# Optimization experiments

Measured on AMD Instinct MI355X. Metric: run time of the kernel, lower is better.

Reference implementation:

```python
import jax, jax.numpy as jnp
import numpy as np

D_MODEL = 512
HEADS = 8
D_FF = 1024
EPS = 1e-5


def layer_norm(x, gamma, beta):
    mu = jnp.mean(x, axis=-1, keepdims=True)
    var = jnp.mean(jnp.square(x - mu), axis=-1, keepdims=True)
    return (x - mu) * jax.lax.rsqrt(var + EPS) * gamma + beta


def mha(q, k, v, mask=None):
    # q,k,v: [B, S, D]; no input/output projections in the original module
    B, Sq, D = q.shape
    Sk = k.shape[1]
    dk = D // HEADS
    qh = q.reshape(B, Sq, HEADS, dk).transpose(0, 2, 1, 3)  # [B,H,Sq,dk]
    kh = k.reshape(B, Sk, HEADS, dk).transpose(0, 2, 1, 3)
    vh = v.reshape(B, Sk, HEADS, dk).transpose(0, 2, 1, 3)
    scores = jnp.einsum('bhqd,bhkd->bhqk', qh, kh) / np.sqrt(dk).astype(q.dtype)
    if mask is not None:
        scores = jnp.where(mask == 0, jnp.asarray(-1e9, scores.dtype), scores)
    attn = jax.nn.softmax(scores, axis=-1)  # dropout is identity in eval mode
    out = jnp.einsum('bhqk,bhkd->bhqd', attn, vh)
    return out.transpose(0, 2, 1, 3).reshape(B, Sq, D)


def setup_inputs() -> dict:
    key = jax.random.key(0)
    ks = jax.random.split(key, 8)
    B, S = 4, 2048
    x = jax.random.normal(ks[0], (B, S, D_MODEL), dtype=jnp.float32)
    encoder_output = jax.random.normal(ks[1], (B, S, D_MODEL), dtype=jnp.float32)
    mask = jax.random.randint(ks[2], (B, 1, S, S), 0, 2, dtype=jnp.int32)
    params = {
        'ln1_g': jnp.ones((D_MODEL,), jnp.float32), 'ln1_b': jnp.zeros((D_MODEL,), jnp.float32),
        'ln2_g': jnp.ones((D_MODEL,), jnp.float32), 'ln2_b': jnp.zeros((D_MODEL,), jnp.float32),
        'ln3_g': jnp.ones((D_MODEL,), jnp.float32), 'ln3_b': jnp.zeros((D_MODEL,), jnp.float32),
        'W1': jax.random.normal(ks[3], (D_MODEL, D_FF), jnp.float32) * (1.0 / np.sqrt(D_MODEL)),
        'b1': jnp.zeros((D_FF,), jnp.float32),
        'W2': jax.random.normal(ks[4], (D_FF, D_MODEL), jnp.float32) * (1.0 / np.sqrt(D_FF)),
        'b2': jnp.zeros((D_MODEL,), jnp.float32),
    }
    return {'x': x, 'encoder_output': encoder_output, 'mask': mask, **params}


def reference(x, encoder_output, mask, ln1_g, ln1_b, ln2_g, ln2_b, ln3_g, ln3_b, W1, b1, W2, b2):
    # pre-norm masked self-attention + residual (dropout = identity, eval mode)
    x1 = layer_norm(x, ln1_g, ln1_b)
    x = x + mha(x1, x1, x1, mask)
    # pre-norm cross-attention + residual
    x1 = layer_norm(x, ln2_g, ln2_b)
    x = x + mha(x1, encoder_output, encoder_output, None)
    # pre-norm FFN + residual
    x1 = layer_norm(x, ln3_g, ln3_b)
    h = jax.nn.relu(x1 @ W1 + b1)
    x = x + (h @ W2 + b2)
    return x
```

## Files before the change

kernel.cpp:

```cpp
#include <hip/hip_runtime.h>
#include <hip/hip_bf16.h>

#define D_MODEL 512
#define HEADS   8
#define DK      64
#define D_FF    1024
#define SEQ     2048
#define BATCH   4
#define NTOK    (BATCH*SEQ)
#define NELEM   (NTOK*D_MODEL)

#define QSCALE  0.18033688011112042f
#define MFIX    40.0f

typedef __attribute__((ext_vector_type(8))) short bf8_t;
typedef __attribute__((ext_vector_type(4))) short bf4_t;
typedef __attribute__((ext_vector_type(4))) float f4_t;

#define GLD16(gp, lp) __builtin_amdgcn_global_load_lds( \
    (const __attribute__((address_space(1))) void*)(gp), \
    (__attribute__((address_space(3))) void*)(lp), 16, 0, 0)

__device__ __forceinline__ float ldf(const void* p, size_t i, int f32) {
    return f32 ? ((const float*)p)[i] : __bfloat162float(((const __hip_bfloat16*)p)[i]);
}
__device__ __forceinline__ short f2bf(float f) {
    union { __hip_bfloat16 h; short s; } u; u.h = __float2bfloat16(f); return u.s;
}
__device__ __forceinline__ float bf2f(short s) {
    return __uint_as_float(((unsigned)(unsigned short)s) << 16);
}
__device__ __forceinline__ unsigned fbits(float f) { return __float_as_uint(f); }

__device__ __forceinline__ float fast_exp2(float x) {
    float r; asm("v_exp_f32 %0, %1" : "=v"(r) : "v"(x)); return r;
}

__global__ void detect_k(const uint4* __restrict__ w, int* __restrict__ flags) {
    __shared__ int found;
    if (threadIdx.x == 0) found = 0;
    __syncthreads();
    int hit = 0;
    for (int i = threadIdx.x; i < 4096; i += 256) {
        uint4 u = w[i];
        if (((u.x & 0x7F80u) == 0x7F80u) || ((u.y & 0x7F80u) == 0x7F80u) ||
            ((u.z & 0x7F80u) == 0x7F80u) || ((u.w & 0x7F80u) == 0x7F80u)) hit = 1;
    }
    if (hit) atomicOr(&found, 1);
    __syncthreads();
    if (threadIdx.x == 0) flags[0] = found ? 1 : 0;
}

__device__ __forceinline__ void transpose_body(const void* src, __hip_bfloat16* dst,
                                               int K, int N, int bxi, int byi, int f32,
                                               __hip_bfloat16 (*t)[33]) {
    int bx = bxi * 32, by = byi * 32;
    int tx = threadIdx.x & 31, ty = threadIdx.x >> 5;
    #pragma unroll
    for (int j = 0; j < 32; j += 8)
        t[ty + j][tx] = __float2bfloat16(ldf(src, (size_t)(by + ty + j) * N + bx + tx, f32));
    __syncthreads();
    #pragma unroll
    for (int j = 0; j < 32; j += 8)
        dst[(size_t)(bx + ty + j) * K + by + tx] = t[tx][ty + j];
}

__global__ __launch_bounds__(256)
void prep_k(const void* __restrict__ enc, const int* __restrict__ mask,
            const void* __restrict__ W1, const void* __restrict__ W2,
            const void* __restrict__ x,
            const void* __restrict__ ln1g, const void* __restrict__ ln1b,
            const void* __restrict__ ln2g, const void* __restrict__ ln2b,
            const void* __restrict__ ln3g, const void* __restrict__ ln3b,
            const void* __restrict__ b1,   const void* __restrict__ b2,
            const int* __restrict__ flagp,
            __hip_bfloat16* __restrict__ bufE, unsigned* __restrict__ mb,
            __hip_bfloat16* __restrict__ W1T, __hip_bfloat16* __restrict__ W2T,
            float* __restrict__ bufX, __hip_bfloat16* __restrict__ bufQ,
            __hip_bfloat16* __restrict__ pbuf) {
    __shared__ __hip_bfloat16 t[32][33];
    int f32 = *flagp;
    int bid = blockIdx.x;
    if (bid < 4096) {
        int i = bid * 256 + threadIdx.x;
        if (f32) {
            float4 a = ((const float4*)enc)[i];
            bf4_t o = { f2bf(a.x), f2bf(a.y), f2bf(a.z), f2bf(a.w) };
            ((bf4_t*)bufE)[i] = o;
        } else {
            ((bf4_t*)bufE)[i] = ((const bf4_t*)enc)[i];
        }
    } else if (bid < 6144) {
        int row  = (bid - 4096) * 4 + (threadIdx.x >> 6);
        int lane = threadIdx.x & 63;
        const int* mr = mask + (size_t)row * SEQ;
        for (int it = 0; it < SEQ/64; it++) {
            unsigned long long bal = __ballot(mr[it*64 + lane] != 0);
            if (lane == 0)  mb[(size_t)row*(SEQ/32) + it*2]     = (unsigned)bal;
            if (lane == 32) mb[(size_t)row*(SEQ/32) + it*2 + 1] = (unsigned)(bal >> 32);
        }
    } else if (bid < 6656) {
        int lb = bid - 6144;
        transpose_body(W1, W1T, D_MODEL, D_FF, lb & 31, lb >> 5, f32, t);
    } else if (bid < 7168) {
        int lb = bid - 6656;
        transpose_body(W2, W2T, D_FF, D_MODEL, lb & 15, lb >> 4, f32, t);
    } else if (bid < 9216) {
        int row  = (bid - 7168) * 4 + (threadIdx.x >> 6);
        int lane = threadIdx.x & 63;
        size_t base = (size_t)row * D_MODEL;
        float v[8];
        if (f32) {
            const float4* xp = (const float4*)((const float*)x + base);
            float4 a = xp[lane], b4 = xp[64 + lane];
            v[0]=a.x; v[1]=a.y; v[2]=a.z; v[3]=a.w;
            v[4]=b4.x; v[5]=b4.y; v[6]=b4.z; v[7]=b4.w;
        } else {
            const bf4_t* xp = (const bf4_t*)((const __hip_bfloat16*)x + base);
            bf4_t a = xp[lane], b4 = xp[64 + lane];
            v[0]=bf2f(a[0]); v[1]=bf2f(a[1]); v[2]=bf2f(a[2]); v[3]=bf2f(a[3]);
            v[4]=bf2f(b4[0]); v[5]=bf2f(b4[1]); v[6]=bf2f(b4[2]); v[7]=bf2f(b4[3]);
        }
        float s = 0.f;
        #pragma unroll
        for (int i = 0; i < 8; i++) s += v[i];
        #pragma unroll
        for (int off = 32; off; off >>= 1) s += __shfl_xor(s, off);
        float mu = s * (1.f / D_MODEL);
        float ss = 0.f;
        #pragma unroll
        for (int i = 0; i < 8; i++) { float d = v[i] - mu; ss += d * d; }
        #pragma unroll
        for (int off = 32; off; off >>= 1) ss += __shfl_xor(ss, off);
        float rstd = rsqrtf(ss * (1.f / D_MODEL) + 1e-5f);
        int c0 = 4*lane, c1 = 256 + 4*lane;
        ((float4*)(bufX + base))[lane]      = make_float4(v[0], v[1], v[2], v[3]);
        ((float4*)(bufX + base))[64 + lane] = make_float4(v[4], v[5], v[6], v[7]);
        bf4_t qa, qb;
        #pragma unroll
        for (int j = 0; j < 4; j++) {
            qa[j] = f2bf((v[j]   - mu) * rstd * ldf(ln1g, c0 + j, f32) + ldf(ln1b, c0 + j, f32));
            qb[j] = f2bf((v[4+j] - mu) * rstd * ldf(ln1g, c1 + j, f32) + ldf(ln1b, c1 + j, f32));
        }
        ((bf4_t*)(bufQ + base))[lane]      = qa;
        ((bf4_t*)(bufQ + base))[64 + lane] = qb;
    } else {
        int i = threadIdx.x;
        for (int k = i; k < 512; k += 256) {
            pbuf[k]        = __float2bfloat16(ldf(ln2g, k, f32));
            pbuf[512 + k]  = __float2bfloat16(ldf(ln2b, k, f32));
            pbuf[1024 + k] = __float2bfloat16(ldf(ln3g, k, f32));
            pbuf[1536 + k] = __float2bfloat16(ldf(ln3b, k, f32));
            pbuf[3072 + k] = __float2bfloat16(ldf(b2, k, f32));
        }
        for (int k = i; k < 1024; k += 256)
            pbuf[2048 + k] = __float2bfloat16(ldf(b1, k, f32));
    }
}

__global__ __launch_bounds__(256)
void layernorm_k(const float* __restrict__ x, const __hip_bfloat16* __restrict__ g,
                 const __hip_bfloat16* __restrict__ b,
                 __hip_bfloat16* __restrict__ y) {
    int row  = blockIdx.x * 4 + (threadIdx.x >> 6);
    int lane = threadIdx.x & 63;
    const float4* xp = (const float4*)(x + (size_t)row * D_MODEL);
    float4 a = xp[lane], b4 = xp[64 + lane];
    float v[8] = {a.x, a.y, a.z, a.w, b4.x, b4.y, b4.z, b4.w};
    float s = 0.f;
    #pragma unroll
    for (int i = 0; i < 8; i++) s += v[i];
    #pragma unroll
    for (int off = 32; off; off >>= 1) s += __shfl_xor(s, off);
    float mu = s * (1.f / D_MODEL);
    float ss = 0.f;
    #pragma unroll
    for (int i = 0; i < 8; i++) { float d = v[i] - mu; ss += d * d; }
    #pragma unroll
    for (int off = 32; off; off >>= 1) ss += __shfl_xor(ss, off);
    float rstd = rsqrtf(ss * (1.f / D_MODEL) + 1e-5f);
    bf4_t ga = ((const bf4_t*)g)[lane], gb = ((const bf4_t*)g)[64 + lane];
    bf4_t ba = ((const bf4_t*)b)[lane], bb = ((const bf4_t*)b)[64 + lane];
    bf4_t ya, yb;
    #pragma unroll
    for (int j = 0; j < 4; j++) {
        ya[j] = f2bf((v[j]   - mu) * rstd * bf2f(ga[j]) + bf2f(ba[j]));
        yb[j] = f2bf((v[4+j] - mu) * rstd * bf2f(gb[j]) + bf2f(bb[j]));
    }
    ((bf4_t*)(y + (size_t)row * D_MODEL))[lane]      = ya;
    ((bf4_t*)(y + (size_t)row * D_MODEL))[64 + lane] = yb;
}

__device__ __forceinline__ bf8_t prescale_q(bf8_t q) {
    bf8_t r;
    #pragma unroll
    for (int j = 0; j < 8; j++) r[j] = f2bf(bf2f(q[j]) * QSCALE);
    return r;
}

template<bool HAS_MASK>
__global__ __launch_bounds__(512, 2)
void attn_mfma_k(const __hip_bfloat16* __restrict__ Q, const __hip_bfloat16* __restrict__ K,
                 const __hip_bfloat16* __restrict__ V, const unsigned* __restrict__ mbits,
                 float* __restrict__ Xout) {
    int bid0 = blockIdx.x;
    int bid = ((bid0 & 7) << 5) | (bid0 >> 3);
    int qt = bid & 7;
    int h  = (bid >> 3) & 7;
    int b  = bid >> 6;
    int q0 = qt * 256;
    int tid  = threadIdx.x;
    int w    = tid >> 6;
    int lane = tid & 63;
    int c    = lane & 15;
    int quad = lane >> 4;

    __shared__ __hip_bfloat16 Kt[4][64 * 64];
    __shared__ __hip_bfloat16 VT[4][64 * 64];
    __shared__ __hip_bfloat16 Pb[8][2][16 * 64];

    bf8_t qf[2][2];
    #pragma unroll
    for (int g = 0; g < 2; g++) {
        const __hip_bfloat16* qrp = Q + ((size_t)(b*SEQ + q0 + 32*w + 16*g + c)) * D_MODEL + h*DK;
        qf[g][0] = prescale_q(*(const bf8_t*)(qrp + quad*8));
        qf[g][1] = prescale_q(*(const bf8_t*)(qrp + 32 + quad*8));
    }

    int kpo[4][2], vpo[4][2];
    #pragma unroll
    for (int t = 0; t < 4; t++)
        #pragma unroll
        for (int kh = 0; kh < 2; kh++) {
            int row = 16*t + c;
            kpo[t][kh] = (row*64 + (((4*kh + quad) ^ (row & 7)) * 8)) * 2;
            vpo[t][kh] = (row*64 + (((4*kh + quad) ^ (row & 7) ^ ((row >> 3) & 7)) * 8)) * 2;
        }

    int vtile = tid >> 8;
    int key0 = ((tid & 255) >> 3) * 2, d0 = (tid & 7) * 8;
    int vtwo[8];
    #pragma unroll
    for (int j = 0; j < 8; j++) {
        int dk = d0 + j;
        int ch = (key0 >> 3) ^ (dk & 7) ^ ((dk >> 3) & 7);
        vtwo[j] = dk*128 + ch*16 + (key0 & 7)*2;
    }

    int krow = tid >> 3;
    int kc8  = ((tid & 7) ^ (krow & 7)) * 8;

    char* pbw[2] = { (char*)&Pb[w][0][0], (char*)&Pb[w][1][0] };
    int pwoff[4], proff[2];
    #pragma unroll
    for (int nt = 0; nt < 4; nt++)
        pwoff[nt] = c*128 + (((2*nt + (quad >> 1)) ^ (c & 7)) * 16) + (quad & 1)*8;
    #pragma unroll
    for (int kh = 0; kh < 2; kh++)
        proff[kh] = c*128 + (((4*kh + quad) ^ (c & 7)) * 16);

    const unsigned* mrp[2] = {nullptr, nullptr};
    if (HAS_MASK) {
        mrp[0] = mbits + (size_t)(b*SEQ + q0 + 32*w + c) * (SEQ/32);
        mrp[1] = mrp[0] + (size_t)16 * (SEQ/32);
    }
    int qsh = quad * 4;

    short onev = (c == 0) ? (short)0x3F80 : (short)0;
    bf8_t ones = {onev, onev, onev, onev, onev, onev, onev, onev};

    f4_t o[2][4];
    #pragma unroll
    for (int g = 0; g < 2; g++)
        #pragma unroll
        for (int mt = 0; mt < 4; mt++) o[g][mt] = (f4_t){0.f,0.f,0.f,0.f};
    f4_t l_acc[2] = {(f4_t){0.f,0.f,0.f,0.f}, (f4_t){0.f,0.f,0.f,0.f}};

    const size_t kvbase = (size_t)b * SEQ * D_MODEL + (size_t)h * DK;

    auto loadV = [&](int k0, bf8_t& r0, bf8_t& r1) {
        const __hip_bfloat16* Vg = V + kvbase + (size_t)(k0 + vtile*64 + key0) * D_MODEL + d0;
        r0 = *(const bf8_t*)Vg;
        r1 = *(const bf8_t*)(Vg + D_MODEL);
    };
    auto stageK = [&](int k0, int bufbase) {
        #pragma unroll
        for (int t = 0; t < 2; t++) {
            const __hip_bfloat16* Kg = K + kvbase + (size_t)(k0 + t*64) * D_MODEL;
            GLD16(Kg + (size_t)krow*D_MODEL + kc8, (char*)&Kt[bufbase + t][0] + (w*64) * 16);
        }
    };
    auto writeV = [&](const bf8_t& r0, const bf8_t& r1, int bufbase) {
        const unsigned* v0u = (const unsigned*)&r0;
        const unsigned* v1u = (const unsigned*)&r1;
        char* vb = (char*)&VT[bufbase + vtile][0];
        #pragma unroll
        for (int dw = 0; dw < 4; dw++) {
            *(unsigned*)(vb + vtwo[2*dw])     = __builtin_amdgcn_perm(v1u[dw], v0u[dw], 0x05040100u);
            *(unsigned*)(vb + vtwo[2*dw + 1]) = __builtin_amdgcn_perm(v1u[dw], v0u[dw], 0x07060302u);
        }
    };

    uint4 pm[2];
    if (HAS_MASK) { pm[0] = *(const uint4*)(mrp[0]); pm[1] = *(const uint4*)(mrp[1]); }
    bf8_t cv0, cv1;
    loadV(0, cv0, cv1);
    stageK(0, 0);
    writeV(cv0, cv1, 0);
    __syncthreads();

    for (int ph = 0; ph < SEQ/128; ph++) {
        int pb = (ph & 1) ? 2 : 0;
        int nb = pb ^ 2;

        uint4 nm[2];
        bf8_t nv0, nv1;
        if (ph < SEQ/128 - 1) {
            int kn = (ph + 1) * 128;
            if (HAS_MASK) {
                nm[0] = *(const uint4*)(mrp[0] + (kn >> 5));
                nm[1] = *(const uint4*)(mrp[1] + (kn >> 5));
            }
            loadV(kn, nv0, nv1);
            stageK(kn, nb);
        }

        #pragma unroll
        for (int t = 0; t < 2; t++) {
            const char* ktb = (const char*)&Kt[pb + t][0];
            const char* vtb = (const char*)&VT[pb + t][0];

            f4_t s[2][4];
            #pragma unroll
            for (int nt = 0; nt < 4; nt++) {
                s[0][nt] = (f4_t){-MFIX,-MFIX,-MFIX,-MFIX};
                s[1][nt] = (f4_t){-MFIX,-MFIX,-MFIX,-MFIX};
            }
            __builtin_amdgcn_s_setprio(1);
            #pragma unroll
            for (int nt = 0; nt < 4; nt++)
                #pragma unroll
                for (int kh = 0; kh < 2; kh++) {
                    bf8_t kf = *(const bf8_t*)(ktb + kpo[nt][kh]);
                    s[0][nt] = __builtin_amdgcn_mfma_f32_16x16x32_bf16(kf, qf[0][kh], s[0][nt], 0, 0, 0);
                    s[1][nt] = __builtin_amdgcn_mfma_f32_16x16x32_bf16(kf, qf[1][kh], s[1][nt], 0, 0, 0);
                }
            __builtin_amdgcn_s_setprio(0);

            #pragma unroll
            for (int g = 0; g < 2; g++) {
                unsigned wq0 = 0xffffffffu, wq1 = 0xffffffffu;
                if (HAS_MASK) {
                    wq0 = (t ? pm[g].z : pm[g].x) >> qsh;
                    wq1 = (t ? pm[g].w : pm[g].y) >> qsh;
                }
                #pragma unroll
                for (int nt = 0; nt < 4; nt++) {
                    #pragma unroll
                    for (int r = 0; r < 4; r++) {
                        float p = fast_exp2(s[g][nt][r]);
                        if (HAS_MASK) {
                            unsigned sel = (nt < 2) ? wq0 : wq1;
                            if (!((sel >> ((nt & 1)*16 + r)) & 1u)) p = 0.f;
                        }
                        s[g][nt][r] = p;
                    }
                    unsigned pk0 = __builtin_amdgcn_perm(fbits(s[g][nt][1]), fbits(s[g][nt][0]), 0x07060302u);
                    unsigned pk1 = __builtin_amdgcn_perm(fbits(s[g][nt][3]), fbits(s[g][nt][2]), 0x07060302u);
                    *(uint2*)(pbw[g] + pwoff[nt]) = make_uint2(pk0, pk1);
                }
            }

            __builtin_amdgcn_s_setprio(1);
            #pragma unroll
            for (int kh = 0; kh < 2; kh++) {
                bf8_t pfA = *(const bf8_t*)(pbw[0] + proff[kh]);
                bf8_t pfB = *(const bf8_t*)(pbw[1] + proff[kh]);
                l_acc[0] = __builtin_amdgcn_mfma_f32_16x16x32_bf16(ones, pfA, l_acc[0], 0, 0, 0);
                l_acc[1] = __builtin_amdgcn_mfma_f32_16x16x32_bf16(ones, pfB, l_acc[1], 0, 0, 0);
                #pragma unroll
                for (int mt = 0; mt < 4; mt++) {
                    bf8_t vf = *(const bf8_t*)(vtb + vpo[mt][kh]);
                    o[0][mt] = __builtin_amdgcn_mfma_f32_16x16x32_bf16(vf, pfA, o[0][mt], 0, 0, 0);
                    o[1][mt] = __builtin_amdgcn_mfma_f32_16x16x32_bf16(vf, pfB, o[1][mt], 0, 0, 0);
                }
            }
            __builtin_amdgcn_s_setprio(0);
        }

        if (ph < SEQ/128 - 1) {
            writeV(nv0, nv1, nb);
            if (HAS_MASK) { pm[0] = nm[0]; pm[1] = nm[1]; }
        }
        __syncthreads();
    }

    #pragma unroll
    for (int g = 0; g < 2; g++) {
        float lq = __shfl(l_acc[g][0], c);
        float il = 1.f / fmaxf(lq, 1e-35f);
        size_t rb = ((size_t)(b*SEQ + q0 + 32*w + 16*g + c)) * D_MODEL + h*DK;
        #pragma unroll
        for (int mt = 0; mt < 4; mt++) {
            float4* xp = (float4*)(Xout + rb + 16*mt + quad*4);
            float4 x4 = *xp;
            x4.x += o[g][mt][0] * il;
            x4.y += o[g][mt][1] * il;
            x4.z += o[g][mt][2] * il;
            x4.w += o[g][mt][3] * il;
            *xp = x4;
        }
    }
}

__global__ __launch_bounds__(256, 2)
void gemm_relu_k(const __hip_bfloat16* __restrict__ A, const __hip_bfloat16* __restrict__ BT,
                 const __hip_bfloat16* __restrict__ bias,
                 __hip_bfloat16* __restrict__ C, int Ksz, int Nsz) {
    __shared__ __hip_bfloat16 As[2][128 * 64];
    __shared__ __hip_bfloat16 Bs[2][128 * 64];
    int tid  = threadIdx.x;
    int w    = tid >> 6;
    int c    = tid & 15;
    int quad = (tid >> 4) & 3;
    int wy = w >> 1, wx = w & 1;
    int lin = blockIdx.y * gridDim.x + blockIdx.x;
    int swz = ((lin & 7) << 6) | (lin >> 3);
    int r0 = (swz >> 3) * 128, c0 = (swz & 7) * 128;

    f4_t acc[4][4];
    #pragma unroll
    for (int i = 0; i < 4; i++)
        #pragma unroll
        for (int j = 0; j < 4; j++) acc[i][j] = (f4_t){0.f,0.f,0.f,0.f};

    auto stage = [&](int k0, int bi) {
        #pragma unroll
        for (int i = 0; i < 4; i++) {
            int idx = i*256 + tid;
            int row = idx >> 3, c8 = idx & 7;
            GLD16(A  + (size_t)(r0 + row) * Ksz + k0 + ((c8 ^ (row & 7)) * 8),
                  (char*)&As[bi][0] + (size_t)(i*256 + w*64) * 16);
            GLD16(BT + (size_t)(c0 + row) * Ksz + k0 + ((c8 ^ (row & 7)) * 8),
                  (char*)&Bs[bi][0] + (size_t)(i*256 + w*64) * 16);
        }
    };

    stage(0, 0);
    __syncthreads();
    int nk = Ksz >> 6;
    for (int ks = 0; ks < nk; ks++) {
        int bi = ks & 1;
        if (ks + 1 < nk) stage((ks + 1) << 6, bi ^ 1);

        #pragma unroll
        for (int kh = 0; kh < 2; kh++) {
            bf8_t af[4], bf[4];
            #pragma unroll
            for (int mt = 0; mt < 4; mt++) {
                int row = wy*64 + mt*16 + c;
                af[mt] = *(const bf8_t*)&As[bi][row*64 + (((kh*4 + quad) ^ (row & 7)) * 8)];
            }
            #pragma unroll
            for (int nt = 0; nt < 4; nt++) {
                int row = wx*64 + nt*16 + c;
                bf[nt] = *(const bf8_t*)&Bs[bi][row*64 + (((kh*4 + quad) ^ (row & 7)) * 8)];
            }
            #pragma unroll
            for (int mt = 0; mt < 4; mt++)
                #pragma unroll
                for (int nt = 0; nt < 4; nt++)
                    acc[mt][nt] = __builtin_amdgcn_mfma_f32_16x16x32_bf16(af[mt], bf[nt], acc[mt][nt], 0, 0, 0);
        }
        __syncthreads();
    }

    #pragma unroll
    for (int mt = 0; mt < 4; mt++)
        #pragma unroll
        for (int nt = 0; nt < 4; nt++) {
            int col = c0 + wx*64 + nt*16 + c;
            float bv = __bfloat162float(bias[col]);
            #pragma unroll
            for (int r = 0; r < 4; r++) {
                int m = r0 + wy*64 + mt*16 + quad*4 + r;
                C[(size_t)m * Nsz + col] = __float2bfloat16(fmaxf(acc[mt][nt][r] + bv, 0.f));
            }
        }
}

__global__ __launch_bounds__(256, 2)
void gemm_out_k(const __hip_bfloat16* __restrict__ A, const __hip_bfloat16* __restrict__ BT,
                const __hip_bfloat16* __restrict__ bias, const float* __restrict__ resid,
                const int* __restrict__ flagp, void* __restrict__ out, int Ksz, int Nsz) {
    int f32 = *flagp;
    __shared__ __hip_bfloat16 As[2][128 * 64];
    __shared__ __hip_bfloat16 Bs[2][64 * 64];
    int tid  = threadIdx.x;
    int w    = tid >> 6;
    int c    = tid & 15;
    int quad = (tid >> 4) & 3;
    int lin = blockIdx.y * gridDim.x + blockIdx.x;
    int swz = ((lin & 7) << 6) | (lin >> 3);
    int r0 = (swz >> 3) * 128, c0 = (swz & 7) * 64;

    f4_t acc[2][4];
    #pragma unroll
    for (int i = 0; i < 2; i++)
        #pragma unroll
        for (int j = 0; j < 4; j++) acc[i][j] = (f4_t){0.f,0.f,0.f,0.f};

    auto stage = [&](int k0, int bi) {
        #pragma unroll
        for (int i = 0; i < 4; i++) {
            int idx = i*256 + tid;
            int row = idx >> 3, c8 = idx & 7;
            GLD16(A + (size_t)(r0 + row) * Ksz + k0 + ((c8 ^ (row & 7)) * 8),
                  (char*)&As[bi][0] + (size_t)(i*256 + w*64) * 16);
        }
        #pragma unroll
        for (int i = 0; i < 2; i++) {
            int idx = i*256 + tid;
            int row = idx >> 3, c8 = idx & 7;
            GLD16(BT + (size_t)(c0 + row) * Ksz + k0 + ((c8 ^ (row & 7)) * 8),
                  (char*)&Bs[bi][0] + (size_t)(i*256 + w*64) * 16);
        }
    };

    stage(0, 0);
    __syncthreads();
    int nk = Ksz >> 6;
    for (int ks = 0; ks < nk; ks++) {
        int bi = ks & 1;
        if (ks + 1 < nk) stage((ks + 1) << 6, bi ^ 1);

        #pragma unroll
        for (int kh = 0; kh < 2; kh++) {
            bf8_t af[2], bf[4];
            #pragma unroll
            for (int mt = 0; mt < 2; mt++) {
                int row = w*32 + mt*16 + c;
                af[mt] = *(const bf8_t*)&As[bi][row*64 + (((kh*4 + quad) ^ (row & 7)) * 8)];
            }
            #pragma unroll
            for (int nt = 0; nt < 4; nt++) {
                int row = nt*16 + c;
                bf[nt] = *(const bf8_t*)&Bs[bi][row*64 + (((kh*4 + quad) ^ (row & 7)) * 8)];
            }
            #pragma unroll
            for (int mt = 0; mt < 2; mt++)
                #pragma unroll
                for (int nt = 0; nt < 4; nt++)
                    acc[mt][nt] = __builtin_amdgcn_mfma_f32_16x16x32_bf16(af[mt], bf[nt], acc[mt][nt], 0, 0, 0);
        }
        __syncthreads();
    }

    #pragma unroll
    for (int mt = 0; mt < 2; mt++)
        #pragma unroll
        for (int nt = 0; nt < 4; nt++) {
            int col = c0 + nt*16 + c;
            float bv = __bfloat162float(bias[col]);
            #pragma unroll
            for (int r = 0; r < 4; r++) {
                int m = r0 + w*32 + mt*16 + quad*4 + r;
                float v = acc[mt][nt][r] + bv + resid[(size_t)m * Nsz + col];
                if (f32) ((float*)out)[(size_t)m * Nsz + col] = v;
                else     ((__hip_bfloat16*)out)[(size_t)m * Nsz + col] = __float2bfloat16(v);
            }
        }
}

extern "C" void kernel_launch(void* const* d_in, const int* in_sizes, int n_in,
                              void* d_out, int out_size, void* d_ws, size_t ws_size,
                              hipStream_t stream) {
    const void* x    = d_in[0];
    const void* enc  = d_in[1];
    const int*  mask = (const int*)d_in[2];
    const void* ln1g = d_in[3];
    const void* ln1b = d_in[4];
    const void* ln2g = d_in[5];
    const void* ln2b = d_in[6];
    const void* ln3g = d_in[7];
    const void* ln3b = d_in[8];
    const void* W1   = d_in[9];
    const void* b1   = d_in[10];
    const void* W2   = d_in[11];
    const void* b2   = d_in[12];

    char* ws = (char*)d_ws;
    float*          bufX  = (float*)ws;
    __hip_bfloat16* bufQ  = (__hip_bfloat16*)(ws + (16u<<20));
    __hip_bfloat16* bufE  = (__hip_bfloat16*)(ws + (24u<<20));
    __hip_bfloat16* bufH  = (__hip_bfloat16*)(ws + (32u<<20));
    __hip_bfloat16* W1T   = (__hip_bfloat16*)(ws + (48u<<20));
    __hip_bfloat16* W2T   = (__hip_bfloat16*)(ws + (49u<<20));
    unsigned*       mbits = (unsigned*)(ws + (50u<<20));
    int*            flags = (int*)(ws + (52u<<20));
    __hip_bfloat16* pbuf  = (__hip_bfloat16*)(ws + (52u<<20) + 4096);

    dim3 blk(256);
    dim3 ablk(512);
    detect_k<<<1, blk, 0, stream>>>((const uint4*)x, flags);
    prep_k<<<9217, blk, 0, stream>>>(enc, mask, W1, W2, x, ln1g, ln1b,
                                     ln2g, ln2b, ln3g, ln3b, b1, b2, flags,
                                     bufE, mbits, W1T, W2T, bufX, bufQ, pbuf);

    attn_mfma_k<true><<<BATCH*HEADS*(SEQ/256), ablk, 0, stream>>>(bufQ, bufQ, bufQ, mbits, bufX);
    layernorm_k<<<NTOK/4, blk, 0, stream>>>(bufX, pbuf, pbuf + 512, bufQ);
    attn_mfma_k<false><<<BATCH*HEADS*(SEQ/256), ablk, 0, stream>>>(bufQ, bufE, bufE, nullptr, bufX);
    layernorm_k<<<NTOK/4, blk, 0, stream>>>(bufX, pbuf + 1024, pbuf + 1536, bufQ);
    gemm_relu_k<<<dim3(D_FF/128, NTOK/128), blk, 0, stream>>>(bufQ, W1T, pbuf + 2048, bufH, D_MODEL, D_FF);
    gemm_out_k<<<dim3(D_MODEL/64, NTOK/128), blk, 0, stream>>>(bufH, W2T, pbuf + 3072, bufX, flags, d_out, D_FF, D_MODEL);
}
```

Measured before the change: 326.2 us.

## Split attention keys into two halves and combine partials in fused LayerNorm

Each attention head and query tile is now processed by two blocks, each covering half of the key range, so the grid doubles from 256 to 512 blocks. Each block writes an unnormalized partial output and its row sums, which suits a fixed-max softmax. The LayerNorm kernel then adds the two partials, divides by the summed denominators, adds the residual, writes back x and normalizes. Per-phase key tiles shrink from 128 to 64 and shared buffers are halved, allowing 4 blocks per SM. The cost is extra fp32 partial-output traffic and fewer MFMAs between barriers.

```diff
diff --git a/kernel.cpp b/kernel.cpp
--- a/kernel.cpp
+++ b/kernel.cpp
@@ -12,6 +12,7 @@
 
 #define QSCALE  0.18033688011112042f
 #define MFIX    40.0f
+#define KSPLIT  1024
 
 typedef __attribute__((ext_vector_type(8))) short bf8_t;
 typedef __attribute__((ext_vector_type(4))) short bf4_t;
@@ -159,14 +160,28 @@
 }
 
 __global__ __launch_bounds__(256)
-void layernorm_k(const float* __restrict__ x, const __hip_bfloat16* __restrict__ g,
-                 const __hip_bfloat16* __restrict__ b,
-                 __hip_bfloat16* __restrict__ y) {
+void lnc_k(float* __restrict__ x, const float* __restrict__ O1, const float* __restrict__ O2,
+           const float* __restrict__ L,
+           const __hip_bfloat16* __restrict__ g, const __hip_bfloat16* __restrict__ b,
+           __hip_bfloat16* __restrict__ y) {
     int row  = blockIdx.x * 4 + (threadIdx.x >> 6);
     int lane = threadIdx.x & 63;
-    const float4* xp = (const float4*)(x + (size_t)row * D_MODEL);
-    float4 a = xp[lane], b4 = xp[64 + lane];
-    float v[8] = {a.x, a.y, a.z, a.w, b4.x, b4.y, b4.z, b4.w};
+    size_t base = (size_t)row * D_MODEL;
+    float4 a   = ((const float4*)(x + base))[lane];
+    float4 b4  = ((const float4*)(x + base))[64 + lane];
+    float4 o1a = ((const float4*)(O1 + base))[lane];
+    float4 o1b = ((const float4*)(O1 + base))[64 + lane];
+    float4 o2a = ((const float4*)(O2 + base))[lane];
+    float4 o2b = ((const float4*)(O2 + base))[64 + lane];
+    int h0 = lane >> 4, h1 = 4 + (lane >> 4);
+    float la = 1.f / fmaxf(L[(size_t)row*HEADS + h0] + L[(size_t)NTOK*HEADS + row*HEADS + h0], 1e-35f);
+    float lb = 1.f / fmaxf(L[(size_t)row*HEADS + h1] + L[(size_t)NTOK*HEADS + row*HEADS + h1], 1e-35f);
+    float v[8] = { a.x + (o1a.x + o2a.x)*la, a.y + (o1a.y + o2a.y)*la,
+                   a.z + (o1a.z + o2a.z)*la, a.w + (o1a.w + o2a.w)*la,
+                   b4.x + (o1b.x + o2b.x)*lb, b4.y + (o1b.y + o2b.y)*lb,
+                   b4.z + (o1b.z + o2b.z)*lb, b4.w + (o1b.w + o2b.w)*lb };
+    ((float4*)(x + base))[lane]      = make_float4(v[0], v[1], v[2], v[3]);
+    ((float4*)(x + base))[64 + lane] = make_float4(v[4], v[5], v[6], v[7]);
     float s = 0.f;
     #pragma unroll
     for (int i = 0; i < 8; i++) s += v[i];
@@ -187,8 +202,8 @@
         ya[j] = f2bf((v[j]   - mu) * rstd * bf2f(ga[j]) + bf2f(ba[j]));
         yb[j] = f2bf((v[4+j] - mu) * rstd * bf2f(gb[j]) + bf2f(bb[j]));
     }
-    ((bf4_t*)(y + (size_t)row * D_MODEL))[lane]      = ya;
-    ((bf4_t*)(y + (size_t)row * D_MODEL))[64 + lane] = yb;
+    ((bf4_t*)(y + base))[lane]      = ya;
+    ((bf4_t*)(y + base))[64 + lane] = yb;
 }
 
 __device__ __forceinline__ bf8_t prescale_q(bf8_t q) {
@@ -199,15 +214,16 @@
 }
 
 template<bool HAS_MASK>
-__global__ __launch_bounds__(512, 2)
+__global__ __launch_bounds__(512, 4)
 void attn_mfma_k(const __hip_bfloat16* __restrict__ Q, const __hip_bfloat16* __restrict__ K,
                  const __hip_bfloat16* __restrict__ V, const unsigned* __restrict__ mbits,
-                 float* __restrict__ Xout) {
+                 float* __restrict__ O1, float* __restrict__ O2, float* __restrict__ Lp) {
     int bid0 = blockIdx.x;
-    int bid = ((bid0 & 7) << 5) | (bid0 >> 3);
-    int qt = bid & 7;
-    int h  = (bid >> 3) & 7;
-    int b  = bid >> 6;
+    int bid = ((bid0 & 7) << 6) | (bid0 >> 3);
+    int split = bid & 1;
+    int qt = (bid >> 1) & 7;
+    int h  = (bid >> 4) & 7;
+    int b  = bid >> 7;
     int q0 = qt * 256;
     int tid  = threadIdx.x;
     int w    = tid >> 6;
@@ -215,8 +231,8 @@
     int c    = lane & 15;
     int quad = lane >> 4;
 
-    __shared__ __hip_bfloat16 Kt[4][64 * 64];
-    __shared__ __hip_bfloat16 VT[4][64 * 64];
+    __shared__ __hip_bfloat16 Kt[2][64 * 64];
+    __shared__ __hip_bfloat16 VT[2][64 * 64];
     __shared__ __hip_bfloat16 Pb[8][2][16 * 64];
 
     bf8_t qf[2][2];
@@ -237,7 +253,6 @@
             vpo[t][kh] = (row*64 + (((4*kh + quad) ^ (row & 7) ^ ((row >> 3) & 7)) * 8)) * 2;
         }
 
-    int vtile = tid >> 8;
     int key0 = ((tid & 255) >> 3) * 2, d0 = (tid & 7) * 8;
     int vtwo[8];
     #pragma unroll
@@ -261,7 +276,7 @@
 
     const unsigned* mrp[2] = {nullptr, nullptr};
     if (HAS_MASK) {
-        mrp[0] = mbits + (size_t)(b*SEQ + q0 + 32*w + c) * (SEQ/32);
+        mrp[0] = mbits + (size_t)(b*SEQ + q0 + 32*w + c) * (SEQ/32) + split*(KSPLIT/32);
         mrp[1] = mrp[0] + (size_t)16 * (SEQ/32);
     }
     int qsh = quad * 4;
@@ -276,24 +291,22 @@
         for (int mt = 0; mt < 4; mt++) o[g][mt] = (f4_t){0.f,0.f,0.f,0.f};
     f4_t l_acc[2] = {(f4_t){0.f,0.f,0.f,0.f}, (f4_t){0.f,0.f,0.f,0.f}};
 
-    const size_t kvbase = (size_t)b * SEQ * D_MODEL + (size_t)h * DK;
+    const size_t kvbase = (size_t)b * SEQ * D_MODEL + (size_t)h * DK
+                        + (size_t)split * KSPLIT * D_MODEL;
 
     auto loadV = [&](int k0, bf8_t& r0, bf8_t& r1) {
-        const __hip_bfloat16* Vg = V + kvbase + (size_t)(k0 + vtile*64 + key0) * D_MODEL + d0;
+        const __hip_bfloat16* Vg = V + kvbase + (size_t)(k0 + key0) * D_MODEL + d0;
         r0 = *(const bf8_t*)Vg;
         r1 = *(const bf8_t*)(Vg + D_MODEL);
     };
-    auto stageK = [&](int k0, int bufbase) {
-        #pragma unroll
-        for (int t = 0; t < 2; t++) {
-            const __hip_bfloat16* Kg = K + kvbase + (size_t)(k0 + t*64) * D_MODEL;
-            GLD16(Kg + (size_t)krow*D_MODEL + kc8, (char*)&Kt[bufbase + t][0] + (w*64) * 16);
-        }
+    auto stageK = [&](int k0, int bi) {
+        const __hip_bfloat16* Kg = K + kvbase + (size_t)k0 * D_MODEL;
+        GLD16(Kg + (size_t)krow*D_MODEL + kc8, (char*)&Kt[bi][0] + (w*64) * 16);
     };
-    auto writeV = [&](const bf8_t& r0, const bf8_t& r1, int bufbase) {
+    auto writeV = [&](const bf8_t& r0, const bf8_t& r1, int bi) {
         const unsigned* v0u = (const unsigned*)&r0;
         const unsigned* v1u = (const unsigned*)&r1;
-        char* vb = (char*)&VT[bufbase + vtile][0];
+        char* vb = (char*)&VT[bi][0];
         #pragma unroll
         for (int dw = 0; dw < 4; dw++) {
             *(unsigned*)(vb + vtwo[2*dw])     = __builtin_amdgcn_perm(v1u[dw], v0u[dw], 0x05040100u);
@@ -301,34 +314,34 @@
         }
     };
 
-    uint4 pm[2];
-    if (HAS_MASK) { pm[0] = *(const uint4*)(mrp[0]); pm[1] = *(const uint4*)(mrp[1]); }
+    uint2 pm[2];
+    if (HAS_MASK) { pm[0] = *(const uint2*)(mrp[0]); pm[1] = *(const uint2*)(mrp[1]); }
     bf8_t cv0, cv1;
-    loadV(0, cv0, cv1);
+    if (tid < 256) loadV(0, cv0, cv1);
     stageK(0, 0);
-    writeV(cv0, cv1, 0);
+    if (tid < 256) writeV(cv0, cv1, 0);
     __syncthreads();
 
-    for (int ph = 0; ph < SEQ/128; ph++) {
-        int pb = (ph & 1) ? 2 : 0;
-        int nb = pb ^ 2;
-
-        uint4 nm[2];
+    const int NPH = KSPLIT / 64;
+    for (int ph = 0; ph < NPH; ph++) {
+        int bi = ph & 1;
+        int ni = bi ^ 1;
+
+        uint2 nm[2];
         bf8_t nv0, nv1;
-        if (ph < SEQ/128 - 1) {
-            int kn = (ph + 1) * 128;
+        if (ph < NPH - 1) {
+            int kn = (ph + 1) * 64;
             if (HAS_MASK) {
-                nm[0] = *(const uint4*)(mrp[0] + (kn >> 5));
-                nm[1] = *(const uint4*)(mrp[1] + (kn >> 5));
-            }
-            loadV(kn, nv0, nv1);
-            stageK(kn, nb);
-        }
-
-        #pragma unroll
-        for (int t = 0; t < 2; t++) {
-            const char* ktb = (const char*)&Kt[pb + t][0];
-            const char* vtb = (const char*)&VT[pb + t][0];
+                nm[0] = *(const uint2*)(mrp[0] + (kn >> 5));
+                nm[1] = *(const uint2*)(mrp[1] + (kn >> 5));
+            }
+            if (tid < 256) loadV(kn, nv0, nv1);
+            stageK(kn, ni);
+        }
+
+        {
+            const char* ktb = (const char*)&Kt[bi][0];
+            const char* vtb = (const char*)&VT[bi][0];
 
             f4_t s[2][4];
             #pragma unroll
@@ -351,8 +364,8 @@
             for (int g = 0; g < 2; g++) {
                 unsigned wq0 = 0xffffffffu, wq1 = 0xffffffffu;
                 if (HAS_MASK) {
-                    wq0 = (t ? pm[g].z : pm[g].x) >> qsh;
-                    wq1 = (t ? pm[g].w : pm[g].y) >> qsh;
+                    wq0 = pm[g].x >> qsh;
+                    wq1 = pm[g].y >> qsh;
                 }
                 #pragma unroll
                 for (int nt = 0; nt < 4; nt++) {
@@ -388,28 +401,24 @@
             __builtin_amdgcn_s_setprio(0);
         }
 
-        if (ph < SEQ/128 - 1) {
-            writeV(nv0, nv1, nb);
+        if (ph < NPH - 1) {
+            if (tid < 256) writeV(nv0, nv1, ni);
             if (HAS_MASK) { pm[0] = nm[0]; pm[1] = nm[1]; }
         }
         __syncthreads();
     }
 
+    float* Op = split ? O2 : O1;
     #pragma unroll
     for (int g = 0; g < 2; g++) {
-        float lq = __shfl(l_acc[g][0], c);
-        float il = 1.f / fmaxf(lq, 1e-35f);
-        size_t rb = ((size_t)(b*SEQ + q0 + 32*w + 16*g + c)) * D_MODEL + h*DK;
-        #pragma unroll
-        for (int mt = 0; mt < 4; mt++) {
-            float4* xp = (float4*)(Xout + rb + 16*mt + quad*4);
-            float4 x4 = *xp;
-            x4.x += o[g][mt][0] * il;
-            x4.y += o[g][mt][1] * il;
-            x4.z += o[g][mt][2] * il;
-            x4.w += o[g][mt][3] * il;
-            *xp = x4;
-        }
+        size_t row = (size_t)(b*SEQ + q0 + 32*w + 16*g + c);
+        if (quad == 0)
+            Lp[(size_t)split * NTOK * HEADS + row * HEADS + h] = l_acc[g][0];
+        size_t rb = row * D_MODEL + h*DK;
+        #pragma unroll
+        for (int mt = 0; mt < 4; mt++)
+            *(float4*)(Op + rb + 16*mt + quad*4) =
+                make_float4(o[g][mt][0], o[g][mt][1], o[g][mt][2], o[g][mt][3]);
     }
 }
 
@@ -599,6 +608,9 @@
     unsigned*       mbits = (unsigned*)(ws + (50u<<20));
     int*            flags = (int*)(ws + (52u<<20));
     __hip_bfloat16* pbuf  = (__hip_bfloat16*)(ws + (52u<<20) + 4096);
+    float*          bufO1 = (float*)(ws + (53u<<20));
+    float*          bufO2 = (float*)bufH;
+    float*          bufL  = (float*)(ws + (69u<<20));
 
     dim3 blk(256);
     dim3 ablk(512);
@@ -607,10 +619,12 @@
                                      ln2g, ln2b, ln3g, ln3b, b1, b2, flags,
                                      bufE, mbits, W1T, W2T, bufX, bufQ, pbuf);
 
-    attn_mfma_k<true><<<BATCH*HEADS*(SEQ/256), ablk, 0, stream>>>(bufQ, bufQ, bufQ, mbits, bufX);
-    layernorm_k<<<NTOK/4, blk, 0, stream>>>(bufX, pbuf, pbuf + 512, bufQ);
-    attn_mfma_k<false><<<BATCH*HEADS*(SEQ/256), ablk, 0, stream>>>(bufQ, bufE, bufE, nullptr, bufX);
-    layernorm_k<<<NTOK/4, blk, 0, stream>>>(bufX, pbuf + 1024, pbuf + 1536, bufQ);
+    attn_mfma_k<true><<<BATCH*HEADS*(SEQ/256)*2, ablk, 0, stream>>>(bufQ, bufQ, bufQ, mbits,
+                                                                    bufO1, bufO2, bufL);
+    lnc_k<<<NTOK/4, blk, 0, stream>>>(bufX, bufO1, bufO2, bufL, pbuf, pbuf + 512, bufQ);
+    attn_mfma_k<false><<<BATCH*HEADS*(SEQ/256)*2, ablk, 0, stream>>>(bufQ, bufE, bufE, nullptr,
+                                                                     bufO1, bufO2, bufL);
+    lnc_k<<<NTOK/4, blk, 0, stream>>>(bufX, bufO1, bufO2, bufL, pbuf + 1024, pbuf + 1536, bufQ);
     gemm_relu_k<<<dim3(D_FF/128, NTOK/128), blk, 0, stream>>>(bufQ, W1T, pbuf + 2048, bufH, D_MODEL, D_FF);
     gemm_out_k<<<dim3(D_MODEL/64, NTOK/128), blk, 0, stream>>>(bufH, W2T, pbuf + 3072, bufX, flags, d_out, D_FF, D_MODEL);
 }
```

Result: slower. 382.1 us (+17.1%).
